# Kernel tuning notes

Measured on AMD Instinct MI355X. Metric: run time of the kernel, lower is better.

Reference implementation:

```python
import jax, jax.numpy as jnp
import numpy as np

EPS = 1e-4          # self.epsilon
STENCIL = 24        # fixed neighbor count


def _apply_G(x, coeffs, neighbors, N):
    """SpMV: y_i = G_ii * x_i + sum_j G_ij * x_{nbr[i,j]}.
    x: [B,N,1], coeffs: [B,N,25], neighbors: [B,N,24] (>=N means invalid)."""
    B = x.shape[0]
    mask = neighbors < N                                   # [B,N,24]
    safe = jnp.where(mask, neighbors, 0)
    x2 = x[..., 0]                                         # [B,N]
    x_nbrs = jnp.take_along_axis(x2, safe.reshape(B, -1), axis=1)
    x_nbrs = x_nbrs.reshape(B, -1, STENCIL) * mask.astype(x.dtype)
    res = x2 * coeffs[:, :, 0] + (x_nbrs * coeffs[:, :, 1:]).sum(axis=2)
    return res[..., None]                                  # [B,N,1]


def _apply_GT(x, coeffs, neighbors, N):
    """Transpose SpMV (scatter-add): y_{nbr[i,j]} += G_ij * x_i."""
    B = x.shape[0]
    mask = neighbors < N
    tgt = jnp.where(mask, neighbors, 0)                    # safe targets; masked vals are 0
    vals = (x * coeffs[:, :, 1:]) * mask.astype(x.dtype)   # [B,N,24]
    res = x[..., 0] * coeffs[:, :, 0]                      # [B,N]
    res = jax.vmap(lambda r, t, v: r.at[t].add(v))(
        res, tgt.reshape(B, -1), vals.reshape(B, -1))
    return res[..., None]                                  # [B,N,1]


def setup_inputs() -> dict:
    key = jax.random.key(0)
    kG, kAd, kAo, kw, kn = jax.random.split(key, 5)
    B, N = 2, 262144
    G_coeffs = jax.random.normal(kG, (B, N, 25), dtype=jnp.float32)
    A_diag = jax.random.normal(kAd, (B, N, 1), dtype=jnp.float32)
    A_off = jax.random.normal(kAo, (B, N, STENCIL), dtype=jnp.float32)
    w = jax.random.normal(kw, (B, N, 1), dtype=jnp.float32)
    valid_mask = jnp.ones((B, N, 1), dtype=jnp.float32)
    neighbors = jax.random.randint(kn, (B, N, STENCIL), 0, 270000, dtype=jnp.int64)
    return {"G_coeffs": G_coeffs, "A_diag": A_diag, "A_off": A_off,
            "w": w, "valid_mask": valid_mask, "neighbors": neighbors}


def reference(G_coeffs, A_diag, A_off, w, valid_mask, neighbors):
    B, N, _ = G_coeffs.shape
    active = valid_mask.sum()
    norm_A = (jnp.abs(A_diag).sum() + jnp.abs(A_off).sum()) / (active * 25 + 1e-6)
    # single probe vector (num_probe_vectors = 1)
    wm = w * valid_mask                                    # probe, masked
    u = _apply_GT(wm, G_coeffs, neighbors, N)
    v = _apply_G(u, G_coeffs, neighbors, N) + EPS * wm
    A_coeffs = jnp.concatenate([A_diag, A_off], axis=2)    # [B,N,25]
    y = _apply_G(v, A_coeffs, neighbors, N)
    z = y / (norm_A + 1e-8)
    diff = (z - wm) * valid_mask
    return (diff ** 2).sum() / (valid_mask.sum() + 1e-6)
```

## Files before the change

kernel.cpp:

```cpp
#include <hip/hip_runtime.h>
#include <stdint.h>

#define STENCIL 24
#define EPS_F 1e-4f
#define BLK 256
#define NXCD 8

#define NODE_N 262144
#define BIN_NODES 2048
#define LBINS 128
#define NBINS 256
#define BIN_CAP_G 49152

#define S_THREADS 512
#define S_EPT 8
#define EDGES_PER_BLOCK (S_THREADS * S_EPT)

typedef int   i32x2 __attribute__((ext_vector_type(2)));

template <typename T>
static __device__ __forceinline__ T ntload(const T* p) {
    return __builtin_nontemporal_load(p);
}

static __device__ __forceinline__ int get_xcc_id() {
    int x;
    asm volatile("s_getreg_b32 %0, hwreg(HW_REG_XCC_ID)" : "=s"(x));
    return x & (NXCD - 1);
}

__device__ __forceinline__ float wave_reduce_f32(float v) {
    #pragma unroll
    for (int off = 32; off > 0; off >>= 1)
        v += __shfl_down(v, off, 64);
    return v;
}

__device__ __forceinline__ void block_reduce5(float v[5], float out[5]) {
    __shared__ float sw[4][5];
    #pragma unroll
    for (int c = 0; c < 5; ++c) v[c] = wave_reduce_f32(v[c]);
    if ((threadIdx.x & 63) == 0) {
        #pragma unroll
        for (int c = 0; c < 5; ++c) sw[threadIdx.x >> 6][c] = v[c];
    }
    __syncthreads();
    if (threadIdx.x == 0) {
        #pragma unroll
        for (int c = 0; c < 5; ++c)
            out[c] = sw[0][c] + sw[1][c] + sw[2][c] + sw[3][c];
    }
}

__global__ __launch_bounds__(S_THREADS)
void k_sortscatter(const float* __restrict__ G, const float* __restrict__ w,
                   const float* __restrict__ mask, const int* __restrict__ nbr,
                   float* __restrict__ u, int* __restrict__ binCnt,
                   int2* __restrict__ pairs) {
    __shared__ int2 rec[EDGES_PER_BLOCK];
    __shared__ int hist[LBINS], incl[LBINS], excl[LBINS], pos[LBINS], gb[LBINS];
    int tid = threadIdx.x;
    if (tid < LBINS) hist[tid] = 0;
    __syncthreads();

    long long blockStart = (long long)blockIdx.x * EDGES_PER_BLOCK;
    long long t0 = blockStart + (long long)tid * S_EPT;

    int nb[S_EPT];
    const int4* p4 = (const int4*)(nbr + t0);
    #pragma unroll
    for (int q = 0; q < S_EPT / 4; ++q) {
        int4 x = p4[q];
        nb[q*4] = x.x; nb[q*4+1] = x.y; nb[q*4+2] = x.z; nb[q*4+3] = x.w;
    }
    #pragma unroll
    for (int e = 0; e < S_EPT; ++e) {
        unsigned n = (unsigned)nb[e];
        if (n < (unsigned)NODE_N) atomicAdd(&hist[n >> 11], 1);
    }
    __syncthreads();

    if (tid < LBINS) incl[tid] = hist[tid];
    __syncthreads();
    for (int d = 1; d < LBINS; d <<= 1) {
        int x = 0;
        if (tid < LBINS && tid >= d) x = incl[tid - d];
        __syncthreads();
        if (tid < LBINS) incl[tid] += x;
        __syncthreads();
    }
    int batchBase = (blockStart >= (long long)NODE_N * STENCIL) ? LBINS : 0;
    if (tid < LBINS) {
        int h = hist[tid];
        int ex = incl[tid] - h;
        excl[tid] = ex;
        pos[tid]  = ex;
        gb[tid]   = h ? atomicAdd(&binCnt[batchBase + tid], h) : 0;
    }
    __syncthreads();

    long long i0 = t0 / STENCIL;
    long long i1 = (t0 + S_EPT - 1) / STENCIL;
    float wm0 = w[i0] * mask[i0];
    float wm1 = (i1 != i0) ? w[i1] * mask[i1] : wm0;
    long long i = i0;
    int j = (int)(t0 - i0 * STENCIL);
    #pragma unroll
    for (int e = 0; e < S_EPT; ++e) {
        float wm = (i == i0) ? wm0 : wm1;
        if (j == 0) u[i] = wm * G[i * 25];
        unsigned n = (unsigned)nb[e];
        if (n < (unsigned)NODE_N) {
            int b = (int)(n >> 11);
            float val = wm * G[i * 25 + 1 + j];
            int lp = atomicAdd(&pos[b], 1);
            rec[lp] = make_int2((int)(n & (BIN_NODES - 1)) | (b << 11), __float_as_int(val));
        }
        if (++j == STENCIL) { j = 0; ++i; }
    }
    __syncthreads();

    int tot = incl[LBINS - 1];
    for (int s = tid; s < tot; s += S_THREADS) {
        int2 r = rec[s];
        int b = (r.x >> 11) & (LBINS - 1);
        int dst = gb[b] + (s - excl[b]);
        if (dst < BIN_CAP_G)
            pairs[(long long)(batchBase + b) * BIN_CAP_G + dst] =
                make_int2(r.x & (BIN_NODES - 1), r.y);
    }
}

__global__ __launch_bounds__(1024)
void k_binaccum(const int* __restrict__ binCnt, const int2* __restrict__ pairs,
                float* __restrict__ u) {
    __shared__ float acc[4][BIN_NODES + 1];
    int g = blockIdx.x, tid = threadIdx.x;
    for (int l = tid; l < BIN_NODES; l += 1024) {
        acc[0][l] = 0.f; acc[1][l] = 0.f; acc[2][l] = 0.f; acc[3][l] = 0.f;
    }
    __syncthreads();
    int cnt = binCnt[g]; if (cnt > BIN_CAP_G) cnt = BIN_CAP_G;
    const i32x2* pb = (const i32x2*)(pairs + (long long)g * BIN_CAP_G);
    int rep = tid & 3;
    for (int s = tid; s < cnt; s += 1024) {
        i32x2 r = __builtin_nontemporal_load(pb + s);
        atomicAdd(&acc[rep][r.x], __int_as_float(r.y));
    }
    __syncthreads();
    long long gbase = (long long)(g >> 7) * NODE_N + (long long)(g & (LBINS - 1)) * BIN_NODES;
    for (int l = tid; l < BIN_NODES; l += 1024)
        u[gbase + l] += acc[0][l] + acc[1][l] + acc[2][l] + acc[3][l];
}

__global__ __launch_bounds__(BLK)
void k_v(const float* __restrict__ G, const float* __restrict__ w,
         const float* __restrict__ mask, const int* __restrict__ nbr,
         const float* __restrict__ u, float* __restrict__ v, long long BN) {
    __shared__ float sg[BLK * 25];
    int tid = threadIdx.x;
    long long base = (long long)blockIdx.x * BLK;
    int rows = (int)(((BN - base) < BLK) ? (BN - base) : BLK);
    const float* gsrc = G + base * 25;
    for (int k = tid; k < rows * 25; k += BLK) sg[k] = ntload(gsrc + k);
    __syncthreads();
    if (tid >= rows) return;
    long long i = base + tid;
    const int4* nb4 = (const int4*)(nbr + i * STENCIL);
    int nn[24];
    #pragma unroll
    for (int q = 0; q < 6; ++q) {
        int4 x = nb4[q];
        nn[q*4] = x.x; nn[q*4+1] = x.y; nn[q*4+2] = x.z; nn[q*4+3] = x.w;
    }
    const float* g  = sg + tid * 25;
    const float* ub = u + (i / NODE_N) * (long long)NODE_N;
    float acc = u[i] * g[0] + EPS_F * ntload(w + i) * ntload(mask + i);
    #pragma unroll
    for (int j = 0; j < STENCIL; ++j) {
        int n = nn[j];
        if ((unsigned)n < (unsigned)NODE_N) acc += g[1 + j] * ub[n];
    }
    v[i] = acc;
}

__global__ __launch_bounds__(BLK)
void k_y(const float* __restrict__ Ad, const float* __restrict__ Ao,
         const float* __restrict__ w, const float* __restrict__ mask,
         const int* __restrict__ nbr, const float* __restrict__ v,
         float* __restrict__ py, int nblk, long long BN) {
    __shared__ float sa[BLK * 25];
    int tid = threadIdx.x;
    long long base = (long long)blockIdx.x * BLK;
    int rows = (int)(((BN - base) < BLK) ? (BN - base) : BLK);
    const float* asrc = Ao + base * STENCIL;
    float asum = 0.f;
    for (int k = tid; k < rows * STENCIL; k += BLK) {
        float x = ntload(asrc + k);
        asum += fabsf(x);
        int r = k / STENCIL, c = k - r * STENCIL;
        sa[r * 25 + c] = x;
    }
    __syncthreads();
    float part[5] = {asum, 0.f, 0.f, 0.f, 0.f};
    if (tid < rows) {
        long long i = base + tid;
        const int4* nb4 = (const int4*)(nbr + i * STENCIL);
        int nn[24];
        #pragma unroll
        for (int q = 0; q < 6; ++q) {
            int4 x = nb4[q];
            nn[q*4] = x.x; nn[q*4+1] = x.y; nn[q*4+2] = x.z; nn[q*4+3] = x.w;
        }
        float ad = ntload(Ad + i);
        part[0] += fabsf(ad);
        const float* a  = sa + tid * 25;
        const float* vb = v + (i / NODE_N) * (long long)NODE_N;
        float acc = v[i] * ad;
        #pragma unroll
        for (int j = 0; j < STENCIL; ++j) {
            int n = nn[j];
            if ((unsigned)n < (unsigned)NODE_N) acc += a[j] * vb[n];
        }
        float m = ntload(mask + i);
        float P = acc * m;
        float Q = ntload(w + i) * m * m;
        part[1] = m;
        part[2] = P * P;
        part[3] = P * Q;
        part[4] = Q * Q;
    }
    float out[5];
    block_reduce5(part, out);
    if (tid == 0) {
        #pragma unroll
        for (int c = 0; c < 5; ++c) py[(long long)c * nblk + blockIdx.x] = out[c];
    }
}

__global__ __launch_bounds__(1024)
void k_final(const float* __restrict__ py, int nblk, float* __restrict__ out) {
    __shared__ float sw[16][5];
    __shared__ float res[5];
    float part[5] = {0.f, 0.f, 0.f, 0.f, 0.f};
    for (int t = threadIdx.x; t < nblk; t += 1024) {
        #pragma unroll
        for (int c = 0; c < 5; ++c) part[c] += py[(long long)c * nblk + t];
    }
    #pragma unroll
    for (int c = 0; c < 5; ++c) part[c] = wave_reduce_f32(part[c]);
    if ((threadIdx.x & 63) == 0) {
        #pragma unroll
        for (int c = 0; c < 5; ++c) sw[threadIdx.x >> 6][c] = part[c];
    }
    __syncthreads();
    if (threadIdx.x == 0) {
        #pragma unroll
        for (int c = 0; c < 5; ++c) {
            float r = 0.f;
            for (int k = 0; k < 16; ++k) r += sw[k][c];
            res[c] = r;
        }
        double A   = res[0], act = res[1];
        double a   = res[2], b   = res[3], c2 = res[4];
        double nrm = A / (act * 25.0 + 1e-6) + 1e-8;
        double loss = (a / (nrm * nrm) - 2.0 * b / nrm + c2) / (act + 1e-6);
        out[0] = (float)loss;
    }
}

__global__ void k_init_fb(const float* __restrict__ G, const float* __restrict__ w,
                          const float* __restrict__ mask, float* __restrict__ u, long long BN) {
    long long i = (long long)blockIdx.x * blockDim.x + threadIdx.x;
    if (i < BN) u[i] = w[i] * mask[i] * G[i * 25];
}
__global__ void k_scatter_fb(const float* __restrict__ G, const float* __restrict__ w,
                             const float* __restrict__ mask, const int* __restrict__ nbr,
                             float* __restrict__ ucopy, int N, long long BN) {
    long long t = (long long)blockIdx.x * blockDim.x + threadIdx.x;
    if (t >= BN * STENCIL) return;
    long long i = t / STENCIL;
    int j = (int)(t - i * STENCIL);
    int n = nbr[t];
    if ((unsigned)n >= (unsigned)N) return;
    float wm = w[i] * mask[i];
    float gv = G[i * 25 + 1 + j];
    float* ub = ucopy + (long long)get_xcc_id() * BN + (i / N) * (long long)N;
    __hip_atomic_fetch_add(&ub[n], wm * gv, __ATOMIC_RELAXED, __HIP_MEMORY_SCOPE_WORKGROUP);
}
__global__ void k_usum_fb(const float* __restrict__ ucopy, float* __restrict__ u, long long BN) {
    long long i = (long long)blockIdx.x * blockDim.x + threadIdx.x;
    if (i >= BN) return;
    float acc = u[i];
    #pragma unroll
    for (int c = 0; c < NXCD; ++c) acc += ucopy[(long long)c * BN + i];
    u[i] = acc;
}

extern "C" void kernel_launch(void* const* d_in, const int* in_sizes, int n_in,
                              void* d_out, int out_size, void* d_ws, size_t ws_size,
                              hipStream_t stream) {
    const float* G    = (const float*)d_in[0];
    const float* Ad   = (const float*)d_in[1];
    const float* Ao   = (const float*)d_in[2];
    const float* w    = (const float*)d_in[3];
    const float* mask = (const float*)d_in[4];
    const int*   nbr  = (const int*)d_in[5];

    const long long BN = in_sizes[3];
    const long long nEdges = BN * STENCIL;
    const int nodeBlocks = (int)((BN + BLK - 1) / BLK);

    float* u  = (float*)d_ws;
    float* v  = u + BN;
    float* py = v + BN;
    char*  after_common = (char*)(py + 5LL * nodeBlocks);

    int*  binCnt = (int*)(((uintptr_t)after_common + 15) & ~(uintptr_t)15);
    int2* pairs  = (int2*)(((uintptr_t)(binCnt + NBINS) + 7) & ~(uintptr_t)7);
    size_t need_fast = (size_t)((char*)(pairs + (long long)NBINS * BIN_CAP_G) - (char*)d_ws);

    float* ucopy = (float*)(((uintptr_t)after_common + 15) & ~(uintptr_t)15);

    bool fast = (BN == 2LL * NODE_N) && (nEdges % EDGES_PER_BLOCK == 0) &&
                (ws_size >= need_fast);

    if (fast) {
        hipMemsetAsync(binCnt, 0, NBINS * sizeof(int), stream);
        int gridS = (int)(nEdges / EDGES_PER_BLOCK);
        k_sortscatter<<<gridS, S_THREADS, 0, stream>>>(G, w, mask, nbr, u, binCnt, pairs);
        k_binaccum<<<NBINS, 1024, 0, stream>>>(binCnt, pairs, u);
    } else {
        hipMemsetAsync(ucopy, 0, (size_t)NXCD * BN * sizeof(float), stream);
        int edgeBlocks = (int)((nEdges + BLK - 1) / BLK);
        k_init_fb<<<nodeBlocks, BLK, 0, stream>>>(G, w, mask, u, BN);
        k_scatter_fb<<<edgeBlocks, BLK, 0, stream>>>(G, w, mask, nbr, ucopy, NODE_N, BN);
        k_usum_fb<<<nodeBlocks, BLK, 0, stream>>>(ucopy, u, BN);
    }
    k_v<<<nodeBlocks, BLK, 0, stream>>>(G, w, mask, nbr, u, v, BN);
    k_y<<<nodeBlocks, BLK, 0, stream>>>(Ad, Ao, w, mask, nbr, v, py, nodeBlocks, BN);
    k_final<<<1, 1024, 0, stream>>>(py, nodeBlocks, (float*)d_out);
}
```

Before: 408.5 us.

## Split bin pairs into u16 ids and float values; use atomic-rank histogram and wave scan

The intermediate bin buffer changes from 8-byte (index, value) pairs to a structure of arrays: 16-bit local node ids plus float values. This cuts the bytes written by the sort-scatter kernel and read back by the bin-accumulate kernel. The sort kernel also keeps the rank returned by each histogram atomic and uses it for local placement, which removes the second round of shared atomics. The barrier-heavy 128-entry prefix scan is replaced by a single-wave shuffle scan. The cost is two separate stream writes and reads per edge instead of one, and narrower 2-byte accesses.

```diff
diff --git a/kernel.cpp b/kernel.cpp
--- a/kernel.cpp
+++ b/kernel.cpp
@@ -17,6 +17,7 @@
 #define EDGES_PER_BLOCK (S_THREADS * S_EPT)
 
 typedef int   i32x2 __attribute__((ext_vector_type(2)));
+typedef unsigned short u16;
 
 template <typename T>
 static __device__ __forceinline__ T ntload(const T* p) {
@@ -56,17 +57,20 @@
 void k_sortscatter(const float* __restrict__ G, const float* __restrict__ w,
                    const float* __restrict__ mask, const int* __restrict__ nbr,
                    float* __restrict__ u, int* __restrict__ binCnt,
-                   int2* __restrict__ pairs) {
+                   u16* __restrict__ idbuf, float* __restrict__ valbuf) {
     __shared__ int2 rec[EDGES_PER_BLOCK];
-    __shared__ int hist[LBINS], incl[LBINS], excl[LBINS], pos[LBINS], gb[LBINS];
+    __shared__ int hist[LBINS], excl[LBINS], gb[LBINS];
+    __shared__ int sTot;
     int tid = threadIdx.x;
     if (tid < LBINS) hist[tid] = 0;
     __syncthreads();
 
     long long blockStart = (long long)blockIdx.x * EDGES_PER_BLOCK;
     long long t0 = blockStart + (long long)tid * S_EPT;
+    int batchBase = (blockStart >= (long long)NODE_N * STENCIL) ? LBINS : 0;
 
     int nb[S_EPT];
+    int rk[S_EPT];
     const int4* p4 = (const int4*)(nbr + t0);
     #pragma unroll
     for (int q = 0; q < S_EPT / 4; ++q) {
@@ -76,26 +80,25 @@
     #pragma unroll
     for (int e = 0; e < S_EPT; ++e) {
         unsigned n = (unsigned)nb[e];
-        if (n < (unsigned)NODE_N) atomicAdd(&hist[n >> 11], 1);
-    }
-    __syncthreads();
-
-    if (tid < LBINS) incl[tid] = hist[tid];
-    __syncthreads();
-    for (int d = 1; d < LBINS; d <<= 1) {
-        int x = 0;
-        if (tid < LBINS && tid >= d) x = incl[tid - d];
-        __syncthreads();
-        if (tid < LBINS) incl[tid] += x;
-        __syncthreads();
-    }
-    int batchBase = (blockStart >= (long long)NODE_N * STENCIL) ? LBINS : 0;
-    if (tid < LBINS) {
-        int h = hist[tid];
-        int ex = incl[tid] - h;
-        excl[tid] = ex;
-        pos[tid]  = ex;
-        gb[tid]   = h ? atomicAdd(&binCnt[batchBase + tid], h) : 0;
+        if (n < (unsigned)NODE_N) rk[e] = atomicAdd(&hist[n >> 11], 1);
+    }
+    __syncthreads();
+
+    if (tid < 64) {
+        int b0 = 2 * tid, b1 = 2 * tid + 1;
+        int h0 = hist[b0], h1 = hist[b1];
+        int s = h0 + h1;
+        int v = s;
+        #pragma unroll
+        for (int off = 1; off < 64; off <<= 1) {
+            int t = __shfl_up(v, off, 64);
+            if (tid >= off) v += t;
+        }
+        excl[b0] = v - s;
+        excl[b1] = v - h1;
+        if (tid == 63) sTot = v;
+        gb[b0] = h0 ? atomicAdd(&binCnt[batchBase + b0], h0) : 0;
+        gb[b1] = h1 ? atomicAdd(&binCnt[batchBase + b1], h1) : 0;
     }
     __syncthreads();
 
@@ -113,27 +116,29 @@
         if (n < (unsigned)NODE_N) {
             int b = (int)(n >> 11);
             float val = wm * G[i * 25 + 1 + j];
-            int lp = atomicAdd(&pos[b], 1);
+            int lp = excl[b] + rk[e];
             rec[lp] = make_int2((int)(n & (BIN_NODES - 1)) | (b << 11), __float_as_int(val));
         }
         if (++j == STENCIL) { j = 0; ++i; }
     }
     __syncthreads();
 
-    int tot = incl[LBINS - 1];
+    int tot = sTot;
     for (int s = tid; s < tot; s += S_THREADS) {
         int2 r = rec[s];
         int b = (r.x >> 11) & (LBINS - 1);
         int dst = gb[b] + (s - excl[b]);
-        if (dst < BIN_CAP_G)
-            pairs[(long long)(batchBase + b) * BIN_CAP_G + dst] =
-                make_int2(r.x & (BIN_NODES - 1), r.y);
+        if (dst < BIN_CAP_G) {
+            long long gidx = (long long)(batchBase + b) * BIN_CAP_G + dst;
+            idbuf[gidx]  = (u16)(r.x & (BIN_NODES - 1));
+            valbuf[gidx] = __int_as_float(r.y);
+        }
     }
 }
 
 __global__ __launch_bounds__(1024)
-void k_binaccum(const int* __restrict__ binCnt, const int2* __restrict__ pairs,
-                float* __restrict__ u) {
+void k_binaccum(const int* __restrict__ binCnt, const u16* __restrict__ idbuf,
+                const float* __restrict__ valbuf, float* __restrict__ u) {
     __shared__ float acc[4][BIN_NODES + 1];
     int g = blockIdx.x, tid = threadIdx.x;
     for (int l = tid; l < BIN_NODES; l += 1024) {
@@ -141,11 +146,13 @@
     }
     __syncthreads();
     int cnt = binCnt[g]; if (cnt > BIN_CAP_G) cnt = BIN_CAP_G;
-    const i32x2* pb = (const i32x2*)(pairs + (long long)g * BIN_CAP_G);
+    const u16*   ib = idbuf  + (long long)g * BIN_CAP_G;
+    const float* vb = valbuf + (long long)g * BIN_CAP_G;
     int rep = tid & 3;
     for (int s = tid; s < cnt; s += 1024) {
-        i32x2 r = __builtin_nontemporal_load(pb + s);
-        atomicAdd(&acc[rep][r.x], __int_as_float(r.y));
+        u16   id  = __builtin_nontemporal_load(ib + s);
+        float val = __builtin_nontemporal_load(vb + s);
+        atomicAdd(&acc[rep][id], val);
     }
     __syncthreads();
     long long gbase = (long long)(g >> 7) * NODE_N + (long long)(g & (LBINS - 1)) * BIN_NODES;
@@ -316,9 +323,10 @@
     float* py = v + BN;
     char*  after_common = (char*)(py + 5LL * nodeBlocks);
 
-    int*  binCnt = (int*)(((uintptr_t)after_common + 15) & ~(uintptr_t)15);
-    int2* pairs  = (int2*)(((uintptr_t)(binCnt + NBINS) + 7) & ~(uintptr_t)7);
-    size_t need_fast = (size_t)((char*)(pairs + (long long)NBINS * BIN_CAP_G) - (char*)d_ws);
+    int*   binCnt = (int*)(((uintptr_t)after_common + 15) & ~(uintptr_t)15);
+    float* valbuf = (float*)(((uintptr_t)(binCnt + NBINS) + 15) & ~(uintptr_t)15);
+    u16*   idbuf  = (u16*)(valbuf + (long long)NBINS * BIN_CAP_G);
+    size_t need_fast = (size_t)((char*)(idbuf + (long long)NBINS * BIN_CAP_G) - (char*)d_ws);
 
     float* ucopy = (float*)(((uintptr_t)after_common + 15) & ~(uintptr_t)15);
 
@@ -328,8 +336,8 @@
     if (fast) {
         hipMemsetAsync(binCnt, 0, NBINS * sizeof(int), stream);
         int gridS = (int)(nEdges / EDGES_PER_BLOCK);
-        k_sortscatter<<<gridS, S_THREADS, 0, stream>>>(G, w, mask, nbr, u, binCnt, pairs);
-        k_binaccum<<<NBINS, 1024, 0, stream>>>(binCnt, pairs, u);
+        k_sortscatter<<<gridS, S_THREADS, 0, stream>>>(G, w, mask, nbr, u, binCnt, idbuf, valbuf);
+        k_binaccum<<<NBINS, 1024, 0, stream>>>(binCnt, idbuf, valbuf, u);
     } else {
         hipMemsetAsync(ucopy, 0, (size_t)NXCD * BN * sizeof(float), stream);
         int edgeBlocks = (int)((nEdges + BLK - 1) / BLK);
```

New measurement: 453.9 us. +11.1%, slower.
